# Performance work log

Measured on AMD Instinct MI355X. Metric: run time of the kernel, lower is better.

The kernel has to match this reference:

```python
import jax, jax.numpy as jnp
import numpy as np

F6_E3M2_MAX = 28.0  # max representable e3m2 value
M_TOKENS, K_IN, N_OUT = 256, 4096, 4096


def _quantize_e3m2(w: np.ndarray) -> np.ndarray:
    """Round-to-nearest onto the FP6 e3m2 grid (bias=3, min normal 2^-2, subnormal step 2^-4)."""
    sign = np.sign(w)
    a = np.minimum(np.abs(w), F6_E3M2_MAX)
    e = np.clip(np.floor(np.log2(np.maximum(a, 1e-30))), -2.0, 4.0)
    step = np.exp2(e - 2.0)  # 2 mantissa bits -> 4 steps per octave; subnormal step = 2^-4
    q = np.round(a / step) * step
    return (sign * np.minimum(q, F6_E3M2_MAX)).astype(np.float32)


def setup_inputs() -> dict:
    key = jax.random.key(0)
    k_x, k_w, k_b = jax.random.split(key, 3)
    x = (jax.random.normal(k_x, (M_TOKENS, K_IN), dtype=jnp.float32)).astype(jnp.float16)
    w_fp32 = np.asarray(jax.random.normal(k_w, (N_OUT, K_IN), dtype=jnp.float32)) * 0.02
    # per-row scale as in to_scaled_tc_float6_e3m2
    amax = np.clip(np.abs(w_fp32).max(axis=1), 1e-12, None)
    scale = F6_E3M2_MAX / amax                       # quantization scale
    weight_fp6 = _quantize_e3m2(w_fp32 * scale[:, None])  # values on the e3m2 grid
    scales = jnp.asarray(1.0 / scale, dtype=jnp.float16)  # dequant scale (stored half)
    bias = (jax.random.normal(k_b, (N_OUT,), dtype=jnp.float32) * 0.01).astype(jnp.float16)
    return {
        "x": x,
        "weight_fp6": jnp.asarray(weight_fp6),
        "scales": scales,
        "bias": bias,
    }


def reference(x, weight_fp6, scales, bias):
    # Fused dequant + GEMM: W = weight_fp6 * row_scale; out = x @ W^T + bias
    in_features = weight_fp6.shape[1]
    x2d = x.reshape(-1, in_features).astype(jnp.float16)
    w_deq = weight_fp6 * scales.astype(jnp.float32)[:, None]  # [N, K] fp32
    out = jnp.einsum("mk,nk->mn", x2d.astype(jnp.float32), w_deq,
                     preferred_element_type=jnp.float32)       # fp32 accumulate (split-K sums in fp32)
    out = out.astype(jnp.float16) + bias
    return out.reshape(*x.shape[:-1], weight_fp6.shape[0]).astype(x.dtype)
```

## Files before the change

### kernel.cpp

```cpp
#include <hip/hip_runtime.h>
#include <hip/hip_fp16.h>


typedef __attribute__((ext_vector_type(8))) _Float16 half8;
typedef __attribute__((ext_vector_type(4))) _Float16 half4;
typedef __attribute__((ext_vector_type(2))) __fp16 fp16x2;
typedef __attribute__((ext_vector_type(4))) float f32x4;

constexpr int K  = 4096;
constexpr int N  = 4096;
constexpr int M  = 256;
constexpr int BM = 64;
constexpr int BN = 64;
constexpr int BK = 128;
constexpr int LDH   = BK + 8;
constexpr int TILEH = 64 * LDH;

__device__ __forceinline__ half4 pack4(float4 v) {
    fp16x2 p0 = __builtin_amdgcn_cvt_pkrtz(v.x, v.y);
    fp16x2 p1 = __builtin_amdgcn_cvt_pkrtz(v.z, v.w);
    half4 h;
    h[0] = (_Float16)p0[0]; h[1] = (_Float16)p0[1];
    h[2] = (_Float16)p1[0]; h[3] = (_Float16)p1[1];
    return h;
}

template <int SPL>
__global__ __launch_bounds__(256, 4)
void fp6lin_gemm(const float* __restrict__ X,
                 const float* __restrict__ W,
                 float* __restrict__ P)
{
    constexpr int KSPL = K / SPL;
    constexpr int NTL  = KSPL / BK;
    constexpr int GRID = 4 * 64 * SPL;

    __shared__ __align__(16) _Float16 lds[2 * TILEH];

    const int tid  = (int)threadIdx.x;
    const int lane = tid & 63;
    const int wid  = tid >> 6;
    const int wm   = (wid & 1) * 32;
    const int wn   = (wid >> 1) * 32;

    const int bid = (int)blockIdx.x;
    const int g   = (bid & 7) * (GRID / 8) + (bid >> 3);
    const int bm  = (g & 3) * BM;
    const int sp  = (g >> 2) % SPL;
    const int bn  = ((g >> 2) / SPL) * BN;
    const int kb  = sp * KSPL;

    const float* Xt = X + (size_t)bm * K + kb;
    const float* Wt = W + (size_t)bn * K + kb;

    const int r0 = tid >> 5;
    const int c0 = 4 * (tid & 31);

    const _Float16* pa = lds + (wm + (lane & 15)) * LDH + ((lane >> 4) << 3);
    const _Float16* pb = lds + TILEH + (wn + (lane & 15)) * LDH + ((lane >> 4) << 3);

    f32x4 acc00 = {0.f, 0.f, 0.f, 0.f};
    f32x4 acc10 = acc00, acc01 = acc00, acc11 = acc00;

    for (int t = 0; t < NTL; ++t) {
        if (t) __syncthreads();
        const float* xa = Xt + t * BK;
        const float* wa = Wt + t * BK;
        #pragma unroll
        for (int j = 0; j < 8; ++j) {
            const int row = j * 8 + r0;
            float4 va = *(const float4*)(xa + (size_t)row * K + c0);
            float4 vb = *(const float4*)(wa + (size_t)row * K + c0);
            *(half4*)(lds + row * LDH + c0)         = pack4(va);
            *(half4*)(lds + TILEH + row * LDH + c0) = pack4(vb);
        }
        __syncthreads();

        #pragma unroll
        for (int kk = 0; kk < BK / 32; ++kk) {
            const _Float16* qa = pa + kk * 32;
            const _Float16* qb = pb + kk * 32;
            half8 a0 = *(const half8*)(qa);
            half8 a1 = *(const half8*)(qa + 16 * LDH);
            half8 b0 = *(const half8*)(qb);
            half8 b1 = *(const half8*)(qb + 16 * LDH);
            acc00 = __builtin_amdgcn_mfma_f32_16x16x32_f16(a0, b0, acc00, 0, 0, 0);
            acc10 = __builtin_amdgcn_mfma_f32_16x16x32_f16(a1, b0, acc10, 0, 0, 0);
            acc01 = __builtin_amdgcn_mfma_f32_16x16x32_f16(a0, b1, acc01, 0, 0, 0);
            acc11 = __builtin_amdgcn_mfma_f32_16x16x32_f16(a1, b1, acc11, 0, 0, 0);
        }
    }

    float* Pb = P + (size_t)sp * M * N;
    const int orow = bm + wm + ((lane >> 4) << 2);
    const int ocol = bn + wn + (lane & 15);
    #pragma unroll
    for (int r = 0; r < 4; ++r) {
        Pb[(size_t)(orow + r) * N + ocol]           = acc00[r];
        Pb[(size_t)(orow + r) * N + ocol + 16]      = acc01[r];
        Pb[(size_t)(orow + 16 + r) * N + ocol]      = acc10[r];
        Pb[(size_t)(orow + 16 + r) * N + ocol + 16] = acc11[r];
    }
}

template <int SPL>
__global__ __launch_bounds__(256)
void fp6lin_finalize(const float* __restrict__ P,
                     const float* __restrict__ S,
                     const float* __restrict__ Bi,
                     float* __restrict__ O)
{
    const size_t i = ((size_t)blockIdx.x * 256 + threadIdx.x) * 4;
    const int n = (int)(i & (N - 1));
    float4 v = *(const float4*)(P + i);
    #pragma unroll
    for (int s = 1; s < SPL; ++s) {
        float4 u = *(const float4*)(P + (size_t)s * M * N + i);
        v.x += u.x; v.y += u.y; v.z += u.z; v.w += u.w;
    }
    float4 sc = *(const float4*)(S + n);
    float4 bb = *(const float4*)(Bi + n);
    v.x = (float)(_Float16)((float)(_Float16)(v.x * sc.x) + bb.x);
    v.y = (float)(_Float16)((float)(_Float16)(v.y * sc.y) + bb.y);
    v.z = (float)(_Float16)((float)(_Float16)(v.z * sc.z) + bb.z);
    v.w = (float)(_Float16)((float)(_Float16)(v.w * sc.w) + bb.w);
    *(float4*)(O + i) = v;
}

extern "C" void kernel_launch(void* const* d_in, const int* in_sizes, int n_in,
                              void* d_out, int out_size, void* d_ws, size_t ws_size,
                              hipStream_t stream) {
    const float* x  = (const float*)d_in[0];
    const float* w  = (const float*)d_in[1];
    const float* s  = (const float*)d_in[2];
    const float* bi = (const float*)d_in[3];
    float* o  = (float*)d_out;
    float* ws = (float*)d_ws;

    const size_t slice = (size_t)M * N * sizeof(float);
    const int fin_grid = M * N / 4 / 256;

    if (ws_size >= 4 * slice) {
        fp6lin_gemm<4><<<dim3(4 * 64 * 4), dim3(256), 0, stream>>>(x, w, ws);
        fp6lin_finalize<4><<<dim3(fin_grid), dim3(256), 0, stream>>>(ws, s, bi, o);
    } else if (ws_size >= 2 * slice) {
        fp6lin_gemm<2><<<dim3(4 * 64 * 2), dim3(256), 0, stream>>>(x, w, ws);
        fp6lin_finalize<2><<<dim3(fin_grid), dim3(256), 0, stream>>>(ws, s, bi, o);
    } else {
        fp6lin_gemm<1><<<dim3(4 * 64), dim3(256), 0, stream>>>(x, w, o);
        fp6lin_finalize<1><<<dim3(fin_grid), dim3(256), 0, stream>>>(o, s, bi, o);
    }
}
```

Before: 37.92 us.

## Enlarge GEMM tiles to 128x128 with register-prefetched double-buffered LDS

The GEMM now uses 128x128 output tiles with BK=64 and 512-thread blocks, so each wave computes 4x2 MFMA tiles. This raises operand reuse per LDS load and cuts redundant global reads of X and W. The next K tile is prefetched into registers while the current LDS buffer is consumed, with one barrier per iteration. The grid shrinks to 256 blocks, which may leave CUs underused, and register pressure rises; the small-workspace fallback becomes a naive scalar kernel.

```diff
diff --git a/kernel.cpp b/kernel.cpp
--- a/kernel.cpp
+++ b/kernel.cpp
@@ -3,107 +3,131 @@
 
 
 typedef __attribute__((ext_vector_type(8))) _Float16 half8;
-typedef __attribute__((ext_vector_type(4))) _Float16 half4;
 typedef __attribute__((ext_vector_type(2))) __fp16 fp16x2;
 typedef __attribute__((ext_vector_type(4))) float f32x4;
 
 constexpr int K  = 4096;
 constexpr int N  = 4096;
 constexpr int M  = 256;
-constexpr int BM = 64;
-constexpr int BN = 64;
-constexpr int BK = 128;
-constexpr int LDH   = BK + 8;
-constexpr int TILEH = 64 * LDH;
+constexpr int BM = 128;
+constexpr int BN = 128;
+constexpr int BK = 64;
+constexpr int SPL  = 4;
+constexpr int KSPL = K / SPL;
+constexpr int NT   = KSPL / BK;
+constexpr int LDH  = BK + 8;
+constexpr int OPH  = BM * LDH;
 
-__device__ __forceinline__ half4 pack4(float4 v) {
-    fp16x2 p0 = __builtin_amdgcn_cvt_pkrtz(v.x, v.y);
-    fp16x2 p1 = __builtin_amdgcn_cvt_pkrtz(v.z, v.w);
-    half4 h;
+__device__ __forceinline__ half8 pack8(float4 a, float4 b) {
+    fp16x2 p0 = __builtin_amdgcn_cvt_pkrtz(a.x, a.y);
+    fp16x2 p1 = __builtin_amdgcn_cvt_pkrtz(a.z, a.w);
+    fp16x2 p2 = __builtin_amdgcn_cvt_pkrtz(b.x, b.y);
+    fp16x2 p3 = __builtin_amdgcn_cvt_pkrtz(b.z, b.w);
+    half8 h;
     h[0] = (_Float16)p0[0]; h[1] = (_Float16)p0[1];
     h[2] = (_Float16)p1[0]; h[3] = (_Float16)p1[1];
+    h[4] = (_Float16)p2[0]; h[5] = (_Float16)p2[1];
+    h[6] = (_Float16)p3[0]; h[7] = (_Float16)p3[1];
     return h;
 }
 
-template <int SPL>
-__global__ __launch_bounds__(256, 4)
+__global__ __launch_bounds__(512, 2)
 void fp6lin_gemm(const float* __restrict__ X,
                  const float* __restrict__ W,
                  float* __restrict__ P)
 {
-    constexpr int KSPL = K / SPL;
-    constexpr int NTL  = KSPL / BK;
-    constexpr int GRID = 4 * 64 * SPL;
-
-    __shared__ __align__(16) _Float16 lds[2 * TILEH];
+    __shared__ __align__(16) _Float16 LA[2][OPH];
+    __shared__ __align__(16) _Float16 LB[2][OPH];
 
     const int tid  = (int)threadIdx.x;
     const int lane = tid & 63;
     const int wid  = tid >> 6;
-    const int wm   = (wid & 1) * 32;
+    const int wm   = (wid & 1) * 64;
     const int wn   = (wid >> 1) * 32;
 
-    const int bid = (int)blockIdx.x;
-    const int g   = (bid & 7) * (GRID / 8) + (bid >> 3);
-    const int bm  = (g & 3) * BM;
-    const int sp  = (g >> 2) % SPL;
-    const int bn  = ((g >> 2) / SPL) * BN;
-    const int kb  = sp * KSPL;
+    const int bid   = (int)blockIdx.x;
+    const int xcd   = bid & 7;
+    const int idx   = bid >> 3;
+    const int bm    = (idx & 1) * BM;
+    const int combo = xcd * 16 + (idx >> 1);
+    const int sp    = combo & 3;
+    const int bn    = (combo >> 2) * BN;
+    const int kb    = sp * KSPL;
 
-    const float* Xt = X + (size_t)bm * K + kb;
-    const float* Wt = W + (size_t)bn * K + kb;
+    const int srow = tid >> 2;
+    const int scol = (tid & 3) * 16;
+    const float* xp = X + (size_t)(bm + srow) * K + kb + scol;
+    const float* wp = W + (size_t)(bn + srow) * K + kb + scol;
+    const int stOff = srow * LDH + scol;
 
-    const int r0 = tid >> 5;
-    const int c0 = 4 * (tid & 31);
+    const int paOff = (wm + (lane & 15)) * LDH + ((lane >> 4) << 3);
+    const int pbOff = (wn + (lane & 15)) * LDH + ((lane >> 4) << 3);
 
-    const _Float16* pa = lds + (wm + (lane & 15)) * LDH + ((lane >> 4) << 3);
-    const _Float16* pb = lds + TILEH + (wn + (lane & 15)) * LDH + ((lane >> 4) << 3);
+    f32x4 acc[4][2];
+    #pragma unroll
+    for (int a = 0; a < 4; ++a)
+        #pragma unroll
+        for (int b = 0; b < 2; ++b)
+            acc[a][b] = (f32x4){0.f, 0.f, 0.f, 0.f};
 
-    f32x4 acc00 = {0.f, 0.f, 0.f, 0.f};
-    f32x4 acc10 = acc00, acc01 = acc00, acc11 = acc00;
+    float4 xa0, xa1, xa2, xa3, wa0, wa1, wa2, wa3;
 
-    for (int t = 0; t < NTL; ++t) {
-        if (t) __syncthreads();
-        const float* xa = Xt + t * BK;
-        const float* wa = Wt + t * BK;
-        #pragma unroll
-        for (int j = 0; j < 8; ++j) {
-            const int row = j * 8 + r0;
-            float4 va = *(const float4*)(xa + (size_t)row * K + c0);
-            float4 vb = *(const float4*)(wa + (size_t)row * K + c0);
-            *(half4*)(lds + row * LDH + c0)         = pack4(va);
-            *(half4*)(lds + TILEH + row * LDH + c0) = pack4(vb);
-        }
+#define LOADR(t) do { const float* xq = xp + (t) * BK; const float* wq = wp + (t) * BK; \
+        xa0 = *(const float4*)(xq);      xa1 = *(const float4*)(xq + 4);               \
+        xa2 = *(const float4*)(xq + 8);  xa3 = *(const float4*)(xq + 12);              \
+        wa0 = *(const float4*)(wq);      wa1 = *(const float4*)(wq + 4);               \
+        wa2 = *(const float4*)(wq + 8);  wa3 = *(const float4*)(wq + 12); } while (0)
+#define STORE(bf) do {                                                  \
+        *(half8*)(&LA[bf][stOff])     = pack8(xa0, xa1);                \
+        *(half8*)(&LA[bf][stOff + 8]) = pack8(xa2, xa3);                \
+        *(half8*)(&LB[bf][stOff])     = pack8(wa0, wa1);                \
+        *(half8*)(&LB[bf][stOff + 8]) = pack8(wa2, wa3); } while (0)
+#define COMPUTE(bf) do {                                                \
+        _Pragma("unroll")                                               \
+        for (int kk = 0; kk < 2; ++kk) {                                \
+            half8 af[4]; half8 bf2[2];                                  \
+            _Pragma("unroll")                                           \
+            for (int ar = 0; ar < 4; ++ar)                              \
+                af[ar] = *(const half8*)(&LA[bf][paOff + ar * 16 * LDH + kk * 32]); \
+            _Pragma("unroll")                                           \
+            for (int br = 0; br < 2; ++br)                              \
+                bf2[br] = *(const half8*)(&LB[bf][pbOff + br * 16 * LDH + kk * 32]); \
+            _Pragma("unroll")                                           \
+            for (int ar = 0; ar < 4; ++ar)                              \
+                _Pragma("unroll")                                       \
+                for (int br = 0; br < 2; ++br)                          \
+                    acc[ar][br] = __builtin_amdgcn_mfma_f32_16x16x32_f16(          \
+                        af[ar], bf2[br], acc[ar][br], 0, 0, 0);         \
+        } } while (0)
+
+    LOADR(0);
+    STORE(0);
+    __syncthreads();
+
+    for (int t = 0; t < NT; ++t) {
+        const int tn = (t + 1 < NT) ? t + 1 : t;
+        LOADR(tn);
+        COMPUTE(t & 1);
+        STORE((t + 1) & 1);
         __syncthreads();
-
-        #pragma unroll
-        for (int kk = 0; kk < BK / 32; ++kk) {
-            const _Float16* qa = pa + kk * 32;
-            const _Float16* qb = pb + kk * 32;
-            half8 a0 = *(const half8*)(qa);
-            half8 a1 = *(const half8*)(qa + 16 * LDH);
-            half8 b0 = *(const half8*)(qb);
-            half8 b1 = *(const half8*)(qb + 16 * LDH);
-            acc00 = __builtin_amdgcn_mfma_f32_16x16x32_f16(a0, b0, acc00, 0, 0, 0);
-            acc10 = __builtin_amdgcn_mfma_f32_16x16x32_f16(a1, b0, acc10, 0, 0, 0);
-            acc01 = __builtin_amdgcn_mfma_f32_16x16x32_f16(a0, b1, acc01, 0, 0, 0);
-            acc11 = __builtin_amdgcn_mfma_f32_16x16x32_f16(a1, b1, acc11, 0, 0, 0);
-        }
     }
+#undef LOADR
+#undef STORE
+#undef COMPUTE
 
     float* Pb = P + (size_t)sp * M * N;
     const int orow = bm + wm + ((lane >> 4) << 2);
     const int ocol = bn + wn + (lane & 15);
     #pragma unroll
-    for (int r = 0; r < 4; ++r) {
-        Pb[(size_t)(orow + r) * N + ocol]           = acc00[r];
-        Pb[(size_t)(orow + r) * N + ocol + 16]      = acc01[r];
-        Pb[(size_t)(orow + 16 + r) * N + ocol]      = acc10[r];
-        Pb[(size_t)(orow + 16 + r) * N + ocol + 16] = acc11[r];
-    }
+    for (int ar = 0; ar < 4; ++ar)
+        #pragma unroll
+        for (int br = 0; br < 2; ++br)
+            #pragma unroll
+            for (int r = 0; r < 4; ++r)
+                Pb[(size_t)(orow + ar * 16 + r) * N + ocol + br * 16] = acc[ar][br][r];
 }
 
-template <int SPL>
+template <int SPLT>
 __global__ __launch_bounds__(256)
 void fp6lin_finalize(const float* __restrict__ P,
                      const float* __restrict__ S,
@@ -114,7 +138,7 @@
     const int n = (int)(i & (N - 1));
     float4 v = *(const float4*)(P + i);
     #pragma unroll
-    for (int s = 1; s < SPL; ++s) {
+    for (int s = 1; s < SPLT; ++s) {
         float4 u = *(const float4*)(P + (size_t)s * M * N + i);
         v.x += u.x; v.y += u.y; v.z += u.z; v.w += u.w;
     }
@@ -125,6 +149,19 @@
     v.z = (float)(_Float16)((float)(_Float16)(v.z * sc.z) + bb.z);
     v.w = (float)(_Float16)((float)(_Float16)(v.w * sc.w) + bb.w);
     *(float4*)(O + i) = v;
+}
+
+__global__ __launch_bounds__(256)
+void fp6lin_small(const float* __restrict__ X, const float* __restrict__ W,
+                  const float* __restrict__ S, const float* __restrict__ Bi,
+                  float* __restrict__ O)
+{
+    const int n = (int)blockIdx.x;
+    const int m = (int)threadIdx.x;
+    float s = 0.f;
+    for (int k = 0; k < K; ++k)
+        s += (float)(_Float16)X[(size_t)m * K + k] * (float)(_Float16)W[(size_t)n * K + k];
+    O[(size_t)m * N + n] = (float)(_Float16)((float)(_Float16)(s * S[n]) + Bi[n]);
 }
 
 extern "C" void kernel_launch(void* const* d_in, const int* in_sizes, int n_in,
@@ -138,16 +175,11 @@
     float* ws = (float*)d_ws;
 
     const size_t slice = (size_t)M * N * sizeof(float);
-    const int fin_grid = M * N / 4 / 256;
 
-    if (ws_size >= 4 * slice) {
-        fp6lin_gemm<4><<<dim3(4 * 64 * 4), dim3(256), 0, stream>>>(x, w, ws);
-        fp6lin_finalize<4><<<dim3(fin_grid), dim3(256), 0, stream>>>(ws, s, bi, o);
-    } else if (ws_size >= 2 * slice) {
-        fp6lin_gemm<2><<<dim3(4 * 64 * 2), dim3(256), 0, stream>>>(x, w, ws);
-        fp6lin_finalize<2><<<dim3(fin_grid), dim3(256), 0, stream>>>(ws, s, bi, o);
+    if (ws_size >= SPL * slice) {
+        fp6lin_gemm<<<dim3(2 * 32 * SPL), dim3(512), 0, stream>>>(x, w, ws);
+        fp6lin_finalize<SPL><<<dim3(M * N / 4 / 256), dim3(256), 0, stream>>>(ws, s, bi, o);
     } else {
-        fp6lin_gemm<1><<<dim3(4 * 64), dim3(256), 0, stream>>>(x, w, o);
-        fp6lin_finalize<1><<<dim3(fin_grid), dim3(256), 0, stream>>>(o, s, bi, o);
+        fp6lin_small<<<dim3(N), dim3(M), 0, stream>>>(x, w, s, bi, o);
     }
 }
```

Measured after the change: 40.73 us. 7.4% more time.
